# Kernel optimization log

Hardware: AMD Instinct MI355X
Metric: run time of the kernel (lower is better)

Reference implementation:

```python
import jax, jax.numpy as jnp
import numpy as np

B, N, HID, H = 2, 2048, 2048, 16
DH = HID // H  # 128


def _rope_tables(n, d, base=10000.0):
    inv_freq = 1.0 / (base ** (np.arange(0, d, 2, dtype=np.float32) / d))
    t = np.arange(n, dtype=np.float32)
    freqs = np.outer(t, inv_freq)                 # [N, d/2]
    emb = np.concatenate([freqs, freqs], axis=-1)  # [N, d]
    return jnp.asarray(np.cos(emb)), jnp.asarray(np.sin(emb))


def setup_inputs() -> dict:
    key = jax.random.key(0)
    k1, k2, k3 = jax.random.split(key, 3)
    std = 1.0 / HID ** 0.5
    cos, sin = _rope_tables(N, DH)
    return {
        "hidden_states": jax.random.normal(k1, (B, N, HID), dtype=jnp.float32),
        "cos": cos,
        "sin": sin,
        "w_qkv": (jax.random.truncated_normal(k2, -2.0, 2.0, (3 * HID, HID), jnp.float32) * std),
        "w_o": (jax.random.truncated_normal(k3, -2.0, 2.0, (HID, HID), jnp.float32) * std),
    }


def _rotate_half(x):
    d = x.shape[-1] // 2
    return jnp.concatenate([-x[..., d:], x[..., :d]], axis=-1)


def reference(hidden_states, cos, sin, w_qkv, w_o):
    b, n, _ = hidden_states.shape
    qkv = (hidden_states @ w_qkv.T).reshape(b, n, 3, H, DH)
    q, k, v = qkv[:, :, 0], qkv[:, :, 1], qkv[:, :, 2]  # [B,N,H,DH]
    c = cos[:, None, :]  # [N,1,DH] broadcasts over heads
    s = sin[:, None, :]
    q = q * c + _rotate_half(q) * s
    k = k * c + _rotate_half(k) * s
    scale = 1.0 / jnp.sqrt(jnp.asarray(DH, q.dtype))
    scores = jnp.einsum("bqhd,bkhd->bhqk", q, k) * scale
    attn = jax.nn.softmax(scores, axis=-1)
    out = jnp.einsum("bhqk,bkhd->bqhd", attn, v).reshape(b, n, HID)
    return out @ w_o.T
```

## Files before the change

### kernel.cpp

```cpp
#include <hip/hip_runtime.h>
#include <math.h>

#define NB 2
#define NN 2048
#define HIDDEN 2048
#define NHEAD 16
#define DHEAD 128

typedef __attribute__((ext_vector_type(8))) short bf16x8;
typedef __attribute__((ext_vector_type(4))) float floatx4;

static __device__ __forceinline__ short f2bf(float f) {
    union { float f; unsigned u; } v; v.f = f;
    unsigned r = v.u + 0x7fffu + ((v.u >> 16) & 1u);
    return (short)(r >> 16);
}
static __device__ __forceinline__ void gload_lds16(const short* g, short* l) {
    __builtin_amdgcn_global_load_lds(
        (const __attribute__((address_space(1))) void*)g,
        (__attribute__((address_space(3))) void*)l, 16, 0, 0);
}

__global__ __launch_bounds__(256) void cast_bf16_3(
    const float* __restrict__ a, const float* __restrict__ b, const float* __restrict__ c,
    short* __restrict__ oa, short* __restrict__ ob, short* __restrict__ oc,
    int n4a, int n4b, int n4c)
{
    int i = blockIdx.x * 256 + threadIdx.x;
    const float* s; short* d; int j;
    if (i < n4a) { s = a; d = oa; j = i; }
    else if (i < n4a + n4b) { s = b; d = ob; j = i - n4a; }
    else if (i < n4a + n4b + n4c) { s = c; d = oc; j = i - n4a - n4b; }
    else return;
    float4 v = ((const float4*)s)[j];
    short4 o;
    o.x = f2bf(v.x); o.y = f2bf(v.y); o.z = f2bf(v.z); o.w = f2bf(v.w);
    ((short4*)d)[j] = o;
}

__global__ __launch_bounds__(512, 2) void gemm_qkv_256x128(
    const short* __restrict__ A, const short* __restrict__ Bw,
    const float* __restrict__ cosT, const float* __restrict__ sinT,
    short* __restrict__ Qp, short* __restrict__ Kp, short* __restrict__ Vtp)
{
    __shared__ __align__(16) short AB[49152];

    const int tid = threadIdx.x;
    const int w = tid >> 6;
    const int l = tid & 63;
    const int quad = l >> 4;
    const int l15 = l & 15;
    const int bn = blockIdx.x * 128;
    const int bm = blockIdx.y * 256;
    const int K = HIDDEN;

    const short* src[6];
    int ldst[6];
#pragma unroll
    for (int ld = 0; ld < 2; ++ld) {
        int chunk = ld * 512 + tid;
        int row = chunk >> 3;
        int j = (chunk & 7) ^ (row & 7);
        int coff = j * 8;
        src[ld]     = A + (size_t)(bm + row) * K + coff;
        src[2 + ld] = A + (size_t)(bm + 128 + row) * K + coff;
        ldst[ld]     = chunk * 16;
        ldst[2 + ld] = 16384 + chunk * 16;
    }
    {
        int row = tid >> 3;
        int j = (tid & 7) ^ (row & 7);
        int coff = j * 8;
        src[4] = Bw + (size_t)(bn + row) * K + coff;
        src[5] = Bw + (size_t)(bn + 64 + row) * K + coff;
        ldst[4] = 32768 + tid * 16;
        ldst[5] = 32768 + 8192 + tid * 16;
    }

    const int xj = l15 & 7;
    const int jq0 = ((0 * 4 + quad) ^ xj) * 16;
    const int jq1 = ((1 * 4 + quad) ^ xj) * 16;
    const int arow = (w * 32 + l15) * 128;
    const int brow = 32768 + l15 * 128;

    floatx4 acc[2][8];
#pragma unroll
    for (int i = 0; i < 2; ++i)
#pragma unroll
        for (int j = 0; j < 8; ++j) acc[i][j] = (floatx4){0.f, 0.f, 0.f, 0.f};

#pragma unroll
    for (int i = 0; i < 6; ++i)
        gload_lds16(src[i], (short*)((char*)AB + ldst[i]));

#define STAGE(i) gload_lds16(src[i] + kpf, (short*)((char*)AB + ldst[i] + so))
#define MFMA(d, x, y) d = __builtin_amdgcn_mfma_f32_16x16x32_bf16(x, y, d, 0, 0, 0)

    const int NT = K / 64;
#pragma unroll 1
    for (int t = 0; t < NT; ++t) {
        const int co = (t & 1) * 49152;
        const int so = co ^ 49152;
        int kpf = (t + 1) * 64;
        if (kpf == K) kpf = 0;

        bf16x8 a[2][2], b[4][2];

        asm volatile("s_waitcnt vmcnt(1)" ::: "memory");
        __builtin_amdgcn_s_barrier();
#pragma unroll
        for (int m = 0; m < 2; ++m) {
            a[m][0] = *(const bf16x8*)((const char*)AB + co + arow + m * 2048 + jq0);
            a[m][1] = *(const bf16x8*)((const char*)AB + co + arow + m * 2048 + jq1);
        }
#pragma unroll
        for (int n = 0; n < 4; ++n) {
            b[n][0] = *(const bf16x8*)((const char*)AB + co + brow + n * 2048 + jq0);
            b[n][1] = *(const bf16x8*)((const char*)AB + co + brow + n * 2048 + jq1);
        }
        STAGE(0); STAGE(1); STAGE(2); STAGE(3); STAGE(4);
        __builtin_amdgcn_s_setprio(1);
#pragma unroll
        for (int m = 0; m < 2; ++m)
#pragma unroll
            for (int n = 0; n < 4; ++n) {
                MFMA(acc[m][n], a[m][0], b[n][0]);
                MFMA(acc[m][n], a[m][1], b[n][1]);
            }
        __builtin_amdgcn_s_setprio(0);

        asm volatile("s_waitcnt vmcnt(5)" ::: "memory");
        __builtin_amdgcn_s_barrier();
#pragma unroll
        for (int n = 0; n < 4; ++n) {
            b[n][0] = *(const bf16x8*)((const char*)AB + co + brow + (4 + n) * 2048 + jq0);
            b[n][1] = *(const bf16x8*)((const char*)AB + co + brow + (4 + n) * 2048 + jq1);
        }
        STAGE(5);
        __builtin_amdgcn_s_setprio(1);
#pragma unroll
        for (int m = 0; m < 2; ++m)
#pragma unroll
            for (int n = 0; n < 4; ++n) {
                MFMA(acc[m][4 + n], a[m][0], b[n][0]);
                MFMA(acc[m][4 + n], a[m][1], b[n][1]);
            }
        __builtin_amdgcn_s_setprio(0);
    }
#undef STAGE
#undef MFMA

    asm volatile("s_waitcnt vmcnt(0)" ::: "memory");

    const int which = bn >> 11;
    const int head = (bn >> 7) & (NHEAD - 1);
    const float qsc = (which == 0) ? 0.12751791525f : 1.0f;

#pragma unroll
    for (int m = 0; m < 2; ++m) {
#pragma unroll
        for (int reg = 0; reg < 4; ++reg) {
            int gm = bm + w * 32 + m * 16 + quad * 4 + reg;
            int b2 = gm >> 11, nseq = gm & (NN - 1);
            int bh = b2 * NHEAD + head;
            if (which == 2) {
#pragma unroll
                for (int n = 0; n < 8; ++n) {
                    int d = n * 16 + l15;
                    Vtp[((size_t)bh * DHEAD + d) * NN + nseq] = f2bf(acc[m][n][reg]);
                }
            } else {
                short* dst = (which == 0 ? Qp : Kp) + ((size_t)bh * NN + nseq) * DHEAD;
#pragma unroll
                for (int p = 0; p < 4; ++p) {
                    int d0 = p * 16 + l15;
                    float c = cosT[(size_t)nseq * DHEAD + d0];
                    float s = sinT[(size_t)nseq * DHEAD + d0];
                    float e0 = acc[m][p][reg];
                    float e1 = acc[m][p + 4][reg];
                    dst[d0]      = f2bf((e0 * c - e1 * s) * qsc);
                    dst[d0 + 64] = f2bf((e1 * c + e0 * s) * qsc);
                }
            }
        }
    }
}

__global__ __launch_bounds__(512, 2) void gemm_out_256x128(
    const short* __restrict__ A, const short* __restrict__ Bw,
    float* __restrict__ Cp)
{
    __shared__ __align__(16) short AB[49152];

    const int tid = threadIdx.x;
    const int w = tid >> 6;
    const int l = tid & 63;
    const int quad = l >> 4;
    const int l15 = l & 15;
    const int bn = blockIdx.x * 128;
    const int bm = blockIdx.y * 256;
    const int K = HIDDEN;

    const short* src[6];
    int ldst[6];
#pragma unroll
    for (int ld = 0; ld < 2; ++ld) {
        int chunk = ld * 512 + tid;
        int row = chunk >> 3;
        int j = (chunk & 7) ^ (row & 7);
        int coff = j * 8;
        src[ld]     = A + (size_t)(bm + row) * K + coff;
        src[2 + ld] = A + (size_t)(bm + 128 + row) * K + coff;
        ldst[ld]     = chunk * 16;
        ldst[2 + ld] = 16384 + chunk * 16;
    }
    {
        int row = tid >> 3;
        int j = (tid & 7) ^ (row & 7);
        int coff = j * 8;
        src[4] = Bw + (size_t)(bn + row) * K + coff;
        src[5] = Bw + (size_t)(bn + 64 + row) * K + coff;
        ldst[4] = 32768 + tid * 16;
        ldst[5] = 32768 + 8192 + tid * 16;
    }

    const int xj = l15 & 7;
    const int jq0 = ((0 * 4 + quad) ^ xj) * 16;
    const int jq1 = ((1 * 4 + quad) ^ xj) * 16;
    const int arow = (w * 32 + l15) * 128;
    const int brow = 32768 + l15 * 128;

    floatx4 acc[2][8];
#pragma unroll
    for (int i = 0; i < 2; ++i)
#pragma unroll
        for (int j = 0; j < 8; ++j) acc[i][j] = (floatx4){0.f, 0.f, 0.f, 0.f};

#pragma unroll
    for (int i = 0; i < 6; ++i)
        gload_lds16(src[i], (short*)((char*)AB + ldst[i]));

#define STAGE(i) gload_lds16(src[i] + kpf, (short*)((char*)AB + ldst[i] + so))
#define MFMA(d, x, y) d = __builtin_amdgcn_mfma_f32_16x16x32_bf16(x, y, d, 0, 0, 0)

    const int NT = K / 64;
#pragma unroll 1
    for (int t = 0; t < NT; ++t) {
        const int co = (t & 1) * 49152;
        const int so = co ^ 49152;
        int kpf = (t + 1) * 64;
        if (kpf == K) kpf = 0;

        bf16x8 a[2][2], b[4][2];

        asm volatile("s_waitcnt vmcnt(1)" ::: "memory");
        __builtin_amdgcn_s_barrier();
#pragma unroll
        for (int m = 0; m < 2; ++m) {
            a[m][0] = *(const bf16x8*)((const char*)AB + co + arow + m * 2048 + jq0);
            a[m][1] = *(const bf16x8*)((const char*)AB + co + arow + m * 2048 + jq1);
        }
#pragma unroll
        for (int n = 0; n < 4; ++n) {
            b[n][0] = *(const bf16x8*)((const char*)AB + co + brow + n * 2048 + jq0);
            b[n][1] = *(const bf16x8*)((const char*)AB + co + brow + n * 2048 + jq1);
        }
        STAGE(0); STAGE(1); STAGE(2); STAGE(3); STAGE(4);
        __builtin_amdgcn_s_setprio(1);
#pragma unroll
        for (int m = 0; m < 2; ++m)
#pragma unroll
            for (int n = 0; n < 4; ++n) {
                MFMA(acc[m][n], a[m][0], b[n][0]);
                MFMA(acc[m][n], a[m][1], b[n][1]);
            }
        __builtin_amdgcn_s_setprio(0);

        asm volatile("s_waitcnt vmcnt(5)" ::: "memory");
        __builtin_amdgcn_s_barrier();
#pragma unroll
        for (int n = 0; n < 4; ++n) {
            b[n][0] = *(const bf16x8*)((const char*)AB + co + brow + (4 + n) * 2048 + jq0);
            b[n][1] = *(const bf16x8*)((const char*)AB + co + brow + (4 + n) * 2048 + jq1);
        }
        STAGE(5);
        __builtin_amdgcn_s_setprio(1);
#pragma unroll
        for (int m = 0; m < 2; ++m)
#pragma unroll
            for (int n = 0; n < 4; ++n) {
                MFMA(acc[m][4 + n], a[m][0], b[n][0]);
                MFMA(acc[m][4 + n], a[m][1], b[n][1]);
            }
        __builtin_amdgcn_s_setprio(0);
    }
#undef STAGE
#undef MFMA

    asm volatile("s_waitcnt vmcnt(0)" ::: "memory");

#pragma unroll
    for (int m = 0; m < 2; ++m) {
#pragma unroll
        for (int reg = 0; reg < 4; ++reg) {
            int row = bm + w * 32 + m * 16 + quad * 4 + reg;
            float* crow = Cp + (size_t)row * HIDDEN + bn;
#pragma unroll
            for (int n = 0; n < 8; ++n)
                crow[n * 16 + l15] = acc[m][n][reg];
        }
    }
}

__global__ __launch_bounds__(512, 2) void attn_mfma8(
    const short* __restrict__ Qb, const short* __restrict__ Kb,
    const short* __restrict__ Vt, short* __restrict__ AOb)
{
    __shared__ __align__(16) short Ks[2][64 * 128];
    __shared__ __align__(16) short Vs[2][128 * 64];
    __shared__ __align__(16) short Ps[8][32][72];

    const int tid = threadIdx.x;
    const int w = tid >> 6;
    const int l = tid & 63;
    const int quad = l >> 4;
    const int l15 = l & 15;
    const int bh = blockIdx.y;
    const int qt = blockIdx.x * 256;

    const short* Qg = Qb + (size_t)bh * NN * DHEAD;
    const short* Kg = Kb + (size_t)bh * NN * DHEAD;
    const short* Vg = Vt + (size_t)bh * DHEAD * NN;

    bf16x8 qf[2][4];
#pragma unroll
    for (int mi = 0; mi < 2; ++mi) {
        const short* qrow = Qg + (size_t)(qt + w * 32 + mi * 16 + l15) * DHEAD + quad * 8;
#pragma unroll
        for (int kc = 0; kc < 4; ++kc) qf[mi][kc] = *(const bf16x8*)(qrow + kc * 32);
    }

    const short* ksrc[2]; int kdst[2];
    const short* vsrc[2]; int vdst[2];
#pragma unroll
    for (int rr = 0; rr < 2; ++rr) {
        int s = rr * 512 + tid;
        {
            int row = s >> 4;
            int j = (s & 15) ^ (row & 15);
            ksrc[rr] = Kg + (size_t)row * DHEAD + j * 8;
            kdst[rr] = s * 8;
        }
        {
            int row = s >> 3;
            int c = (s & 7) ^ (row & 7);
            vsrc[rr] = Vg + (size_t)row * NN + c * 8;
            vdst[rr] = s * 8;
        }
    }

    floatx4 of[2][8];
#pragma unroll
    for (int mi = 0; mi < 2; ++mi)
#pragma unroll
        for (int dc = 0; dc < 8; ++dc) of[mi][dc] = (floatx4){0.f, 0.f, 0.f, 0.f};
    float ls[2] = {0.f, 0.f};

#pragma unroll
    for (int rr = 0; rr < 2; ++rr) {
        gload_lds16(ksrc[rr], &Ks[0][0] + kdst[rr]);
        gload_lds16(vsrc[rr], &Vs[0][0] + vdst[rr]);
    }
    asm volatile("s_waitcnt vmcnt(0)" ::: "memory");
    __builtin_amdgcn_s_barrier();

    int cur = 0;
#pragma unroll 1
    for (int kt = 0; kt < NN; kt += 64) {
        if (kt + 64 < NN) {
            const int nxt = cur ^ 1;
#pragma unroll
            for (int rr = 0; rr < 2; ++rr) {
                gload_lds16(ksrc[rr] + (size_t)(kt + 64) * DHEAD, &Ks[nxt][0] + kdst[rr]);
                gload_lds16(vsrc[rr] + (kt + 64), &Vs[nxt][0] + vdst[rr]);
            }
        }
        const short* kb = &Ks[cur][0];
        const short* vb = &Vs[cur][0];

        floatx4 sf[2][4];
#pragma unroll
        for (int n16 = 0; n16 < 4; ++n16) {
            bf16x8 kf[4];
            const short* kbase = kb + (n16 * 16 + l15) * 128;
#pragma unroll
            for (int kc = 0; kc < 4; ++kc)
                kf[kc] = *(const bf16x8*)&kbase[((4 * kc + quad) ^ l15) * 8];
#pragma unroll
            for (int mi = 0; mi < 2; ++mi) {
                floatx4 acc = (floatx4){0.f, 0.f, 0.f, 0.f};
#pragma unroll
                for (int kc = 0; kc < 4; ++kc)
                    acc = __builtin_amdgcn_mfma_f32_16x16x32_bf16(kf[kc], qf[mi][kc], acc, 0, 0, 0);
                sf[mi][n16] = acc;
            }
        }

#pragma unroll
        for (int mi = 0; mi < 2; ++mi)
#pragma unroll
            for (int n16 = 0; n16 < 4; ++n16) {
                float p0 = exp2f(sf[mi][n16][0]);
                float p1 = exp2f(sf[mi][n16][1]);
                float p2 = exp2f(sf[mi][n16][2]);
                float p3 = exp2f(sf[mi][n16][3]);
                ls[mi] += (p0 + p1) + (p2 + p3);
                unsigned u0, u1;
                asm("v_cvt_pk_bf16_f32 %0, %1, %2" : "=v"(u0) : "v"(p0), "v"(p1));
                asm("v_cvt_pk_bf16_f32 %0, %1, %2" : "=v"(u1) : "v"(p2), "v"(p3));
                uint2 uu; uu.x = u0; uu.y = u1;
                *(uint2*)&Ps[w][mi * 16 + l15][n16 * 16 + quad * 4] = uu;
            }

        bf16x8 pa[2][2];
#pragma unroll
        for (int mi = 0; mi < 2; ++mi)
#pragma unroll
            for (int kc = 0; kc < 2; ++kc)
                pa[mi][kc] = *(const bf16x8*)&Ps[w][mi * 16 + l15][kc * 32 + quad * 8];

#pragma unroll
        for (int dc = 0; dc < 8; ++dc) {
            int row = dc * 16 + l15;
#pragma unroll
            for (int kc = 0; kc < 2; ++kc) {
                bf16x8 vf = *(const bf16x8*)&vb[row * 64 + (((kc * 4 + quad) ^ (row & 7)) * 8)];
#pragma unroll
                for (int mi = 0; mi < 2; ++mi)
                    of[mi][dc] = __builtin_amdgcn_mfma_f32_16x16x32_bf16(
                                     pa[mi][kc], vf, of[mi][dc], 0, 0, 0);
            }
        }

        asm volatile("s_waitcnt vmcnt(0)" ::: "memory");
        __builtin_amdgcn_s_barrier();
        cur ^= 1;
    }

    const int b = bh >> 4, h = bh & (NHEAD - 1);
#pragma unroll
    for (int mi = 0; mi < 2; ++mi) {
        float s = ls[mi];
        s += __shfl_xor(s, 16, 64);
        s += __shfl_xor(s, 32, 64);
#pragma unroll
        for (int r = 0; r < 4; ++r) {
            float sr = __shfl(s, quad * 4 + r, 64);
            float inv = 1.0f / sr;
            int row = qt + w * 32 + mi * 16 + quad * 4 + r;
            short* dst = AOb + ((size_t)(b * NN + row)) * HIDDEN + h * DHEAD;
#pragma unroll
            for (int dc = 0; dc < 8; ++dc)
                dst[dc * 16 + l15] = f2bf(of[mi][dc][r] * inv);
        }
    }
}

extern "C" void kernel_launch(void* const* d_in, const int* in_sizes, int n_in,
                              void* d_out, int out_size, void* d_ws, size_t ws_size,
                              hipStream_t stream)
{
    const float* hs = (const float*)d_in[0];
    const float* cosT = (const float*)d_in[1];
    const float* sinT = (const float*)d_in[2];
    const float* wqkv = (const float*)d_in[3];
    const float* wo = (const float*)d_in[4];
    float* out = (float*)d_out;

    const size_t N_HS = (size_t)NB * NN * HIDDEN;
    const size_t N_WQ = (size_t)3 * HIDDEN * HIDDEN;
    const size_t N_WO = (size_t)HIDDEN * HIDDEN;
    const size_t SZ = (size_t)NB * NHEAD * NN * DHEAD;

    short* Ahs   = (short*)d_ws;
    short* Wqkvb = Ahs + N_HS;
    short* Wob   = Wqkvb + N_WQ;
    short* Qb    = Wob + N_WO;
    short* Kb    = Qb + SZ;
    short* Vtb   = Kb + SZ;
    short* AOb   = Vtb + SZ;

    {
        int n4a = (int)(N_HS / 4), n4b = (int)(N_WQ / 4), n4c = (int)(N_WO / 4);
        int total = n4a + n4b + n4c;
        cast_bf16_3<<<(total + 255) / 256, 256, 0, stream>>>(
            hs, wqkv, wo, Ahs, Wqkvb, Wob, n4a, n4b, n4c);
    }
    {
        dim3 grid(3 * HIDDEN / 128, NB * NN / 256);
        gemm_qkv_256x128<<<grid, 512, 0, stream>>>(
            Ahs, Wqkvb, cosT, sinT, Qb, Kb, Vtb);
    }
    {
        dim3 grid(NN / 256, NB * NHEAD);
        attn_mfma8<<<grid, 512, 0, stream>>>(Qb, Kb, Vtb, AOb);
    }
    {
        dim3 grid(HIDDEN / 128, NB * NN / 256);
        gemm_out_256x128<<<grid, 512, 0, stream>>>(AOb, Wob, out);
    }
}
```

Baseline: 382.7 us.

## Triple-buffer K/V tiles in attention and raise wave priority around MFMAs

```diff
diff --git a/kernel.cpp b/kernel.cpp
--- a/kernel.cpp
+++ b/kernel.cpp
@@ -316,8 +316,8 @@
     const short* __restrict__ Qb, const short* __restrict__ Kb,
     const short* __restrict__ Vt, short* __restrict__ AOb)
 {
-    __shared__ __align__(16) short Ks[2][64 * 128];
-    __shared__ __align__(16) short Vs[2][128 * 64];
+    __shared__ __align__(16) short Ks[3][64 * 128];
+    __shared__ __align__(16) short Vs[3][128 * 64];
     __shared__ __align__(16) short Ps[8][32][72];
 
     const int tid = threadIdx.x;
@@ -371,22 +371,29 @@
         gload_lds16(ksrc[rr], &Ks[0][0] + kdst[rr]);
         gload_lds16(vsrc[rr], &Vs[0][0] + vdst[rr]);
     }
-    asm volatile("s_waitcnt vmcnt(0)" ::: "memory");
+#pragma unroll
+    for (int rr = 0; rr < 2; ++rr) {
+        gload_lds16(ksrc[rr] + (size_t)64 * DHEAD, &Ks[1][0] + kdst[rr]);
+        gload_lds16(vsrc[rr] + 64, &Vs[1][0] + vdst[rr]);
+    }
+    asm volatile("s_waitcnt vmcnt(4)" ::: "memory");
     __builtin_amdgcn_s_barrier();
 
-    int cur = 0;
+    const int NT = NN / 64;
 #pragma unroll 1
-    for (int kt = 0; kt < NN; kt += 64) {
-        if (kt + 64 < NN) {
-            const int nxt = cur ^ 1;
+    for (int t = 0; t < NT; ++t) {
+        const int kt = t * 64;
+        const int cb = t % 3;
+        if (t + 2 < NT) {
+            const int sb = (t + 2) % 3;
 #pragma unroll
             for (int rr = 0; rr < 2; ++rr) {
-                gload_lds16(ksrc[rr] + (size_t)(kt + 64) * DHEAD, &Ks[nxt][0] + kdst[rr]);
-                gload_lds16(vsrc[rr] + (kt + 64), &Vs[nxt][0] + vdst[rr]);
-            }
-        }
-        const short* kb = &Ks[cur][0];
-        const short* vb = &Vs[cur][0];
+                gload_lds16(ksrc[rr] + (size_t)(kt + 128) * DHEAD, &Ks[sb][0] + kdst[rr]);
+                gload_lds16(vsrc[rr] + (kt + 128), &Vs[sb][0] + vdst[rr]);
+            }
+        }
+        const short* kb = &Ks[cb][0];
+        const short* vb = &Vs[cb][0];
 
         floatx4 sf[2][4];
 #pragma unroll
@@ -396,6 +403,7 @@
 #pragma unroll
             for (int kc = 0; kc < 4; ++kc)
                 kf[kc] = *(const bf16x8*)&kbase[((4 * kc + quad) ^ l15) * 8];
+            __builtin_amdgcn_s_setprio(1);
 #pragma unroll
             for (int mi = 0; mi < 2; ++mi) {
                 floatx4 acc = (floatx4){0.f, 0.f, 0.f, 0.f};
@@ -404,6 +412,7 @@
                     acc = __builtin_amdgcn_mfma_f32_16x16x32_bf16(kf[kc], qf[mi][kc], acc, 0, 0, 0);
                 sf[mi][n16] = acc;
             }
+            __builtin_amdgcn_s_setprio(0);
         }
 
 #pragma unroll
@@ -435,16 +444,21 @@
 #pragma unroll
             for (int kc = 0; kc < 2; ++kc) {
                 bf16x8 vf = *(const bf16x8*)&vb[row * 64 + (((kc * 4 + quad) ^ (row & 7)) * 8)];
+                __builtin_amdgcn_s_setprio(1);
 #pragma unroll
                 for (int mi = 0; mi < 2; ++mi)
                     of[mi][dc] = __builtin_amdgcn_mfma_f32_16x16x32_bf16(
                                      pa[mi][kc], vf, of[mi][dc], 0, 0, 0);
-            }
-        }
-
-        asm volatile("s_waitcnt vmcnt(0)" ::: "memory");
+                __builtin_amdgcn_s_setprio(0);
+            }
+        }
+
+        if (t + 2 < NT) {
+            asm volatile("s_waitcnt vmcnt(4)" ::: "memory");
+        } else {
+            asm volatile("s_waitcnt vmcnt(0)" ::: "memory");
+        }
         __builtin_amdgcn_s_barrier();
-        cur ^= 1;
     }
 
     const int b = bh >> 4, h = bh & (NHEAD - 1);
```

New measurement: 396.4 us. 3.6% more time.
